# Performance work log

Hardware: AMD Instinct MI355X
Metric: run time of the kernel (lower is better)

The kernel has to match this reference:

```python
import jax, jax.numpy as jnp
import numpy as np
import math

N, T, NS, NO, HID = 256, 1000, 10, 10, 64


def gru_seq(x, Wi, Wh, bi, bh):
    # x: [N,T,D] -> hidden states [N,T,HID] (single-layer GRU, h0 = 0)
    xproj = x @ Wi + bi  # [N,T,3H], precompute input projections
    def step(h, xp):
        hp = h @ Wh + bh
        xr, xz, xn = jnp.split(xp, 3, axis=-1)
        hr, hz, hn = jnp.split(hp, 3, axis=-1)
        r = jax.nn.sigmoid(xr + hr)
        z = jax.nn.sigmoid(xz + hz)
        n = jnp.tanh(xn + r * hn)
        h_new = (1.0 - z) * n + z * h
        return h_new, h_new
    h0 = jnp.zeros((x.shape[0], Wh.shape[0]), x.dtype)
    _, hs = jax.lax.scan(step, h0, jnp.swapaxes(xproj, 0, 1))
    return jnp.swapaxes(hs, 0, 1)


def setup_inputs() -> dict:
    key = jax.random.key(0)
    ks = jax.random.split(key, 12)
    D = NO + NS  # GRU input = concat(y, x_hat)
    s = lambda fan: 1.0 / np.sqrt(fan)
    inp = {
        "Yi_batch": jax.random.normal(ks[0], (N, T, NO), jnp.float32),
        "X_hat_batch": jax.random.normal(ks[1], (N, T, NS), jnp.float32),
        # per-sample observation noise covariance: 0.5*I plus small random diagonal
        "Cw_batch": 0.5 * jnp.eye(NO, dtype=jnp.float32)[None] + jnp.eye(NO)[None] * 0.1 * jax.random.uniform(ks[2], (N, 1, 1), jnp.float32),
        "H": jax.random.normal(ks[3], (NO, NS), jnp.float32) * s(NS),
        "mu_w": jnp.zeros((NO, 1), jnp.float32),
        "Wi": jax.random.normal(ks[4], (D, 3 * HID), jnp.float32) * s(D),
        "Wh": jax.random.normal(ks[5], (HID, 3 * HID), jnp.float32) * s(HID),
        "bi": jnp.zeros((3 * HID,), jnp.float32),
        "bh": jnp.zeros((3 * HID,), jnp.float32),
        "W_mu": jax.random.normal(ks[6], (HID, NS), jnp.float32) * s(HID),
        "b_mu": jnp.zeros((NS,), jnp.float32),
        "W_var": jax.random.normal(ks[7], (HID, NS), jnp.float32) * s(HID),
        "b_var": jnp.zeros((NS,), jnp.float32),
    }
    return inp


def reference(Yi_batch, X_hat_batch, Cw_batch, H, mu_w, Wi, Wh, bi, bh, W_mu, b_mu, W_var, b_var):
    n_obs = Yi_batch.shape[-1]
    Tlen = Yi_batch.shape[1]
    # RNN: mu and (positive) vars per time step
    hs = gru_seq(jnp.concatenate([Yi_batch, X_hat_batch], axis=-1), Wi, Wh, bi, bh)
    mu_prev = hs @ W_mu + b_mu                       # [N,T,NS]
    var_prev = jax.nn.softplus(hs @ W_var + b_var)   # [N,T,NS] diag of L_xt_yt_prev
    # marginal over y: mu_y = H mu_prev + mu_w ; L_y = H diag(var) H^T + Cw
    mu_y = jnp.einsum('ij,ntj->nti', H, mu_prev) + mu_w[:, 0]
    HLH = jnp.einsum('ij,ntj,kj->ntik', H, var_prev, H)   # [N,T,NO,NO]
    L_y = HLH + Cw_batch[:, None]                          # broadcast Cw over time
    e = Yi_batch - mu_y
    # Gaussian log-likelihood via Cholesky (L_y is SPD)
    chol = jnp.linalg.cholesky(L_y)
    logdet = 2.0 * jnp.sum(jnp.log(jnp.diagonal(chol, axis1=-2, axis2=-1)), axis=-1)  # [N,T]
    sol = jnp.linalg.solve(L_y, e[..., None])[..., 0]
    quad = jnp.sum(e * sol, axis=-1)                       # [N,T]
    logprob = (-0.5 * n_obs * Tlen * math.log(2.0 * math.pi)
               - 0.5 * jnp.sum(logdet, axis=1)
               - 0.5 * jnp.sum(quad, axis=1))              # [N]
    return jnp.mean(logprob / (Tlen * n_obs))
```

## Files before the change

kernel.cpp:

```cpp
#include <hip/hip_runtime.h>
#include <math.h>

#define BN 256
#define TT 1000
#define NO 10
#define NS 10
#define HID 64
#define DIN 20
#define G3 192
#define WV 4
#define KW 16
#define GS 8
#define NG 125

__device__ __forceinline__ float bcast(float v, int l) {
    return __int_as_float(__builtin_amdgcn_readlane(__float_as_int(v), l));
}
__device__ __forceinline__ float rcpf(float x) { return __builtin_amdgcn_rcpf(x); }

__global__ __launch_bounds__(256, 1)
void gru_phase1(const float* __restrict__ Yi, const float* __restrict__ Xh,
                const float* __restrict__ Wi, const float* __restrict__ Wh,
                const float* __restrict__ bi, const float* __restrict__ bh,
                const float* __restrict__ Wmu, const float* __restrict__ Wvar,
                float* __restrict__ mv_out) {
    const int n = blockIdx.x;
    const int tid = threadIdx.x;
    const int lane = tid & 63;
    const int w = tid >> 6;
    const int kb = w * KW;

    __shared__ float part[2][5][WV][HID];
    __shared__ float inbuf[2][GS * DIN];
    __shared__ float obuf[2][GS * DIN];

    float whr[KW], whz[KW], whn[KW], wmv[KW];
    float wir[5], wiz[5], win[5];
#pragma unroll
    for (int k = 0; k < KW; ++k) {
        const int kk = kb + k;
        whr[k] = Wh[kk * G3 + lane];
        whz[k] = Wh[kk * G3 + 64 + lane];
        whn[k] = Wh[kk * G3 + 128 + lane];
        float wm = (lane < NS) ? Wmu[kk * NS + lane] : 0.0f;
        float wv = (lane >= NS && lane < 2 * NS) ? Wvar[kk * NS + (lane - NS)] : 0.0f;
        wmv[k] = wm + wv;
    }
#pragma unroll
    for (int k = 0; k < 5; ++k) {
        const int kk = 5 * w + k;
        wir[k] = Wi[kk * G3 + lane];
        wiz[k] = Wi[kk * G3 + 64 + lane];
        win[k] = Wi[kk * G3 + 128 + lane];
    }
    const float b_r  = bi[lane] + bh[lane];
    const float b_z  = bi[64 + lane] + bh[64 + lane];
    const float bx_n = bi[128 + lane];
    const float bh_n = bh[128 + lane];

    const float* ybase = Yi + (size_t)n * TT * NO;
    const float* xbase = Xh + (size_t)n * TT * NS;
    float* obase = mv_out + (size_t)n * TT * DIN;

    const int ibase = ((w >= 2) ? 80 : 0) + (w & 1) * 5;

    if (tid < 160)
        inbuf[0][tid] = (tid < 80) ? ybase[tid] : xbase[tid - 80];
    __syncthreads();

    float h = 0.0f;

#pragma unroll 1
    for (int g = 0; g < NG; ++g) {
        float ld = 0.0f;
        const bool do_ld = (tid < 160) && (g + 1 < NG);
        if (do_ld)
            ld = (tid < 80) ? ybase[(size_t)(g + 1) * 80 + tid]
                            : xbase[(size_t)(g + 1) * 80 + tid - 80];
        const float* ib = inbuf[g & 1];

#pragma unroll
        for (int s = 0; s < GS; ++s) {
            const float* ip = ib + ibase + s * 10;
            const float x0 = ip[0], x1 = ip[1], x2 = ip[2], x3 = ip[3], x4 = ip[4];
            float pr = x0 * wir[0], pz = x0 * wiz[0], px = x0 * win[0];
            pr += x1 * wir[1]; pz += x1 * wiz[1]; px += x1 * win[1];
            pr += x2 * wir[2]; pz += x2 * wiz[2]; px += x2 * win[2];
            pr += x3 * wir[3]; pz += x3 * wiz[3]; px += x3 * win[3];
            pr += x4 * wir[4]; pz += x4 * wiz[4]; px += x4 * win[4];
            float pra = 0, prb = 0, pza = 0, pzb = 0;
            float pna = 0, pnb = 0, pma = 0, pmb = 0;
#pragma unroll
            for (int k = 0; k < 8; ++k) {
                float sv = bcast(h, kb + k);
                pra += sv * whr[k]; pza += sv * whz[k];
                pna += sv * whn[k]; pma += sv * wmv[k];
            }
#pragma unroll
            for (int k = 8; k < KW; ++k) {
                float sv = bcast(h, kb + k);
                prb += sv * whr[k]; pzb += sv * whz[k];
                pnb += sv * whn[k]; pmb += sv * wmv[k];
            }
            const int bufp = s & 1;
            part[bufp][0][w][lane] = pr + pra + prb;
            part[bufp][1][w][lane] = pz + pza + pzb;
            part[bufp][2][w][lane] = px;
            part[bufp][3][w][lane] = pna + pnb;
            part[bufp][4][w][lane] = pma + pmb;
            if (s == GS - 1 && do_ld) inbuf[(g + 1) & 1][tid] = ld;
            __syncthreads();

            float ar = b_r, az = b_z, ax = bx_n, ah = bh_n;
#pragma unroll
            for (int ww = 0; ww < WV; ++ww) {
                ar += part[bufp][0][ww][lane];
                az += part[bufp][1][ww][lane];
                ax += part[bufp][2][ww][lane];
                ah += part[bufp][3][ww][lane];
            }
            if (w == 0) {
                float amv = part[bufp][4][0][lane] + part[bufp][4][1][lane]
                          + part[bufp][4][2][lane] + part[bufp][4][3][lane];
                if (lane < DIN && !(g == 0 && s == 0)) {
                    const int tm1 = 8 * g + s - 1;
                    obuf[(tm1 >> 3) & 1][(tm1 & 7) * DIN + lane] = amv;
                }
            }
            if (s == 1 && g >= 1 && tid < 160)
                obase[(size_t)(g - 1) * 160 + tid] = obuf[(g - 1) & 1][tid];

            float r = rcpf(1.0f + __expf(-ar));
            float z = rcpf(1.0f + __expf(-az));
            float pre = ax + r * ah;
            pre = fminf(fmaxf(pre, -15.0f), 15.0f);
            float e2 = __expf(2.0f * pre);
            float nn = 1.0f - 2.0f * rcpf(e2 + 1.0f);
            h = nn + z * (h - nn);
        }
    }

    {
        float pma = 0, pmb = 0;
#pragma unroll
        for (int k = 0; k < 8; ++k) pma += bcast(h, kb + k) * wmv[k];
#pragma unroll
        for (int k = 8; k < KW; ++k) pmb += bcast(h, kb + k) * wmv[k];
        part[0][4][w][lane] = pma + pmb;
        __syncthreads();
        if (w == 0 && lane < DIN) {
            float amv = part[0][4][0][lane] + part[0][4][1][lane]
                      + part[0][4][2][lane] + part[0][4][3][lane];
            obuf[0][7 * DIN + lane] = amv;
        }
        __syncthreads();
        if (tid < 160)
            obase[(size_t)(NG - 1) * 160 + tid] = obuf[0][tid];
    }
}

__global__ void init_out(float* out) {
    out[0] = -0.918938533204672742f;
}

__global__ __launch_bounds__(256)
void lik_phase2(const float* __restrict__ Yi, const float* __restrict__ Cw,
                const float* __restrict__ Hm, const float* __restrict__ mu_w,
                const float* __restrict__ b_mu, const float* __restrict__ b_var,
                const float* __restrict__ mv_in, float* __restrict__ out) {
    __shared__ float sH[NO * NS];
    __shared__ float smw[NO], sbm[NS], sbv[NS];
    __shared__ float ssum[4];
    const int tid = threadIdx.x;
    if (tid < NO * NS) sH[tid] = Hm[tid];
    if (tid < NO) smw[tid] = mu_w[tid];
    if (tid < NS) { sbm[tid] = b_mu[tid]; sbv[tid] = b_var[tid]; }
    __syncthreads();

    const int gid = blockIdx.x * 256 + tid;
    float contrib = 0.0f;
    if (gid < BN * TT) {
        const int n = gid / TT;
        const float* mv = mv_in + (size_t)gid * DIN;
        float mu[NS], va[NS];
#pragma unroll
        for (int i = 0; i < NS; ++i) {
            mu[i] = mv[i] + sbm[i];
            float x = mv[NS + i] + sbv[i];
            va[i] = (x > 0.0f) ? (x + log1pf(__expf(-x))) : log1pf(__expf(x));
        }
        const float* y = Yi + (size_t)gid * NO;
        float e[NO];
#pragma unroll
        for (int i = 0; i < NO; ++i) {
            float m = smw[i];
#pragma unroll
            for (int j = 0; j < NS; ++j) m += sH[i * NS + j] * mu[j];
            e[i] = y[i] - m;
        }
        float M[NO][NO];
        const float* cw = Cw + (size_t)n * NO * NO;
#pragma unroll
        for (int i = 0; i < NO; ++i)
#pragma unroll
            for (int j = 0; j <= i; ++j) M[i][j] = cw[i * NO + j];
#pragma unroll
        for (int l = 0; l < NS; ++l) {
            float vl = va[l];
            float hv[NO];
#pragma unroll
            for (int i = 0; i < NO; ++i) hv[i] = sH[i * NS + l];
#pragma unroll
            for (int i = 0; i < NO; ++i) {
                float hvi = hv[i] * vl;
#pragma unroll
                for (int j = 0; j <= i; ++j) M[i][j] += hvi * hv[j];
            }
        }
        float logdet = 0.0f;
#pragma unroll
        for (int j = 0; j < NO; ++j) {
            float d = M[j][j];
#pragma unroll
            for (int k = 0; k < j; ++k) d -= M[j][k] * M[j][k];
            logdet += __logf(d);
            float s = sqrtf(d);
            M[j][j] = s;
            float inv = 1.0f / s;
#pragma unroll
            for (int i = j + 1; i < NO; ++i) {
                float v = M[i][j];
#pragma unroll
                for (int k = 0; k < j; ++k) v -= M[i][k] * M[j][k];
                M[i][j] = v * inv;
            }
        }
        float wv[NO];
        float quad = 0.0f;
#pragma unroll
        for (int i = 0; i < NO; ++i) {
            float v = e[i];
#pragma unroll
            for (int k = 0; k < i; ++k) v -= M[i][k] * wv[k];
            wv[i] = v / M[i][i];
            quad += wv[i] * wv[i];
        }
        const float SCALE = 0.5f / ((float)BN * (float)TT * (float)NO);
        contrib = -(logdet + quad) * SCALE;
    }

#pragma unroll
    for (int off = 32; off > 0; off >>= 1) contrib += __shfl_down(contrib, off);
    if ((tid & 63) == 0) ssum[tid >> 6] = contrib;
    __syncthreads();
    if (tid == 0) {
        float s = ssum[0] + ssum[1] + ssum[2] + ssum[3];
        atomicAdd(out, s);
    }
}

extern "C" void kernel_launch(void* const* d_in, const int* in_sizes, int n_in,
                              void* d_out, int out_size, void* d_ws, size_t ws_size,
                              hipStream_t stream) {
    const float* Yi    = (const float*)d_in[0];
    const float* Xh    = (const float*)d_in[1];
    const float* Cw    = (const float*)d_in[2];
    const float* Hm    = (const float*)d_in[3];
    const float* mu_w  = (const float*)d_in[4];
    const float* Wi    = (const float*)d_in[5];
    const float* Wh    = (const float*)d_in[6];
    const float* bi    = (const float*)d_in[7];
    const float* bh    = (const float*)d_in[8];
    const float* W_mu  = (const float*)d_in[9];
    const float* b_mu  = (const float*)d_in[10];
    const float* W_var = (const float*)d_in[11];
    const float* b_var = (const float*)d_in[12];
    float* out = (float*)d_out;
    float* mv  = (float*)d_ws;

    init_out<<<1, 1, 0, stream>>>(out);
    gru_phase1<<<dim3(BN), dim3(256), 0, stream>>>(Yi, Xh, Wi, Wh, bi, bh,
                                                   W_mu, W_var, mv);
    lik_phase2<<<dim3((BN * TT + 255) / 256), dim3(256), 0, stream>>>(
        Yi, Cw, Hm, mu_w, b_mu, b_var, mv, out);
}
```

Before: 632.4 us.

## Pack two GRU samples per 512-thread block and drop tanh clamp

The GRU recurrence kernel now processes two batch samples per workgroup of 8 waves, giving 128 blocks instead of 256, with shared buffers indexed by sub-sample. The aim is to cut the block count so every block fits on the 256 CUs in a single wave, and to let two independent recurrences share each barrier and CU, hiding latency. The clamp on the tanh pre-activation is also removed. The risk is that each barrier now waits on 8 waves, which may lengthen the serial critical path per step. Without the clamp, a large pre-activation makes exp overflow to inf, which the rcp form still handles.

```diff
diff --git a/kernel.cpp b/kernel.cpp
--- a/kernel.cpp
+++ b/kernel.cpp
@@ -12,27 +12,38 @@
 #define KW 16
 #define GS 8
 #define NG 125
+#define SMP 2
 
 __device__ __forceinline__ float bcast(float v, int l) {
     return __int_as_float(__builtin_amdgcn_readlane(__float_as_int(v), l));
 }
 __device__ __forceinline__ float rcpf(float x) { return __builtin_amdgcn_rcpf(x); }
 
-__global__ __launch_bounds__(256, 1)
+__global__
+__attribute__((amdgpu_flat_work_group_size(512, 512), amdgpu_waves_per_eu(2, 2)))
 void gru_phase1(const float* __restrict__ Yi, const float* __restrict__ Xh,
                 const float* __restrict__ Wi, const float* __restrict__ Wh,
                 const float* __restrict__ bi, const float* __restrict__ bh,
                 const float* __restrict__ Wmu, const float* __restrict__ Wvar,
                 float* __restrict__ mv_out) {
-    const int n = blockIdx.x;
     const int tid = threadIdx.x;
     const int lane = tid & 63;
     const int w = tid >> 6;
-    const int kb = w * KW;
-
-    __shared__ float part[2][5][WV][HID];
-    __shared__ float inbuf[2][GS * DIN];
-    __shared__ float obuf[2][GS * DIN];
+    const int ws = w & 3;
+    const int sm = w >> 2;
+    const int kb = ws * KW;
+
+    __shared__ float part[2][5][SMP][WV][HID];
+    __shared__ float inbuf[2][SMP][GS * DIN];
+    __shared__ float obuf[2][SMP][GS * DIN];
+
+    const int sm2 = (tid >= 160) ? 1 : 0;
+    const int lt = tid - 160 * sm2;
+    const bool stg = (tid < 320);
+    const int ns = 2 * blockIdx.x + sm2;
+    const float* ybase = Yi + (size_t)ns * TT * NO;
+    const float* xbase = Xh + (size_t)ns * TT * NS;
+    float* obase = mv_out + (size_t)ns * TT * DIN;
 
     float whr[KW], whz[KW], whn[KW], wmv[KW];
     float wir[5], wiz[5], win[5];
@@ -48,7 +59,7 @@
     }
 #pragma unroll
     for (int k = 0; k < 5; ++k) {
-        const int kk = 5 * w + k;
+        const int kk = 5 * ws + k;
         wir[k] = Wi[kk * G3 + lane];
         wiz[k] = Wi[kk * G3 + 64 + lane];
         win[k] = Wi[kk * G3 + 128 + lane];
@@ -58,14 +69,10 @@
     const float bx_n = bi[128 + lane];
     const float bh_n = bh[128 + lane];
 
-    const float* ybase = Yi + (size_t)n * TT * NO;
-    const float* xbase = Xh + (size_t)n * TT * NS;
-    float* obase = mv_out + (size_t)n * TT * DIN;
-
-    const int ibase = ((w >= 2) ? 80 : 0) + (w & 1) * 5;
-
-    if (tid < 160)
-        inbuf[0][tid] = (tid < 80) ? ybase[tid] : xbase[tid - 80];
+    const int ibase = ((ws >= 2) ? 80 : 0) + (ws & 1) * 5;
+
+    if (stg)
+        inbuf[0][sm2][lt] = (lt < 80) ? ybase[lt] : xbase[lt - 80];
     __syncthreads();
 
     float h = 0.0f;
@@ -73,11 +80,11 @@
 #pragma unroll 1
     for (int g = 0; g < NG; ++g) {
         float ld = 0.0f;
-        const bool do_ld = (tid < 160) && (g + 1 < NG);
+        const bool do_ld = stg && (g + 1 < NG);
         if (do_ld)
-            ld = (tid < 80) ? ybase[(size_t)(g + 1) * 80 + tid]
-                            : xbase[(size_t)(g + 1) * 80 + tid - 80];
-        const float* ib = inbuf[g & 1];
+            ld = (lt < 80) ? ybase[(size_t)(g + 1) * 80 + lt]
+                           : xbase[(size_t)(g + 1) * 80 + (lt - 80)];
+        const float* ib = inbuf[g & 1][sm];
 
 #pragma unroll
         for (int s = 0; s < GS; ++s) {
@@ -103,37 +110,36 @@
                 pnb += sv * whn[k]; pmb += sv * wmv[k];
             }
             const int bufp = s & 1;
-            part[bufp][0][w][lane] = pr + pra + prb;
-            part[bufp][1][w][lane] = pz + pza + pzb;
-            part[bufp][2][w][lane] = px;
-            part[bufp][3][w][lane] = pna + pnb;
-            part[bufp][4][w][lane] = pma + pmb;
-            if (s == GS - 1 && do_ld) inbuf[(g + 1) & 1][tid] = ld;
+            part[bufp][0][sm][ws][lane] = pr + pra + prb;
+            part[bufp][1][sm][ws][lane] = pz + pza + pzb;
+            part[bufp][2][sm][ws][lane] = px;
+            part[bufp][3][sm][ws][lane] = pna + pnb;
+            part[bufp][4][sm][ws][lane] = pma + pmb;
+            if (s == GS - 1 && do_ld) inbuf[(g + 1) & 1][sm2][lt] = ld;
             __syncthreads();
 
             float ar = b_r, az = b_z, ax = bx_n, ah = bh_n;
 #pragma unroll
             for (int ww = 0; ww < WV; ++ww) {
-                ar += part[bufp][0][ww][lane];
-                az += part[bufp][1][ww][lane];
-                ax += part[bufp][2][ww][lane];
-                ah += part[bufp][3][ww][lane];
-            }
-            if (w == 0) {
-                float amv = part[bufp][4][0][lane] + part[bufp][4][1][lane]
-                          + part[bufp][4][2][lane] + part[bufp][4][3][lane];
+                ar += part[bufp][0][sm][ww][lane];
+                az += part[bufp][1][sm][ww][lane];
+                ax += part[bufp][2][sm][ww][lane];
+                ah += part[bufp][3][sm][ww][lane];
+            }
+            if (ws == 0) {
+                float amv = part[bufp][4][sm][0][lane] + part[bufp][4][sm][1][lane]
+                          + part[bufp][4][sm][2][lane] + part[bufp][4][sm][3][lane];
                 if (lane < DIN && !(g == 0 && s == 0)) {
                     const int tm1 = 8 * g + s - 1;
-                    obuf[(tm1 >> 3) & 1][(tm1 & 7) * DIN + lane] = amv;
+                    obuf[(tm1 >> 3) & 1][sm][(tm1 & 7) * DIN + lane] = amv;
                 }
             }
-            if (s == 1 && g >= 1 && tid < 160)
-                obase[(size_t)(g - 1) * 160 + tid] = obuf[(g - 1) & 1][tid];
+            if (s == 1 && g >= 1 && stg)
+                obase[(size_t)(g - 1) * 160 + lt] = obuf[(g - 1) & 1][sm2][lt];
 
             float r = rcpf(1.0f + __expf(-ar));
             float z = rcpf(1.0f + __expf(-az));
             float pre = ax + r * ah;
-            pre = fminf(fmaxf(pre, -15.0f), 15.0f);
             float e2 = __expf(2.0f * pre);
             float nn = 1.0f - 2.0f * rcpf(e2 + 1.0f);
             h = nn + z * (h - nn);
@@ -146,16 +152,16 @@
         for (int k = 0; k < 8; ++k) pma += bcast(h, kb + k) * wmv[k];
 #pragma unroll
         for (int k = 8; k < KW; ++k) pmb += bcast(h, kb + k) * wmv[k];
-        part[0][4][w][lane] = pma + pmb;
+        part[0][4][sm][ws][lane] = pma + pmb;
         __syncthreads();
-        if (w == 0 && lane < DIN) {
-            float amv = part[0][4][0][lane] + part[0][4][1][lane]
-                      + part[0][4][2][lane] + part[0][4][3][lane];
-            obuf[0][7 * DIN + lane] = amv;
+        if (ws == 0 && lane < DIN) {
+            float amv = part[0][4][sm][0][lane] + part[0][4][sm][1][lane]
+                      + part[0][4][sm][2][lane] + part[0][4][sm][3][lane];
+            obuf[0][sm][7 * DIN + lane] = amv;
         }
         __syncthreads();
-        if (tid < 160)
-            obase[(size_t)(NG - 1) * 160 + tid] = obuf[0][tid];
+        if (stg)
+            obase[(size_t)(NG - 1) * 160 + lt] = obuf[0][sm2][lt];
     }
 }
 
@@ -279,8 +285,8 @@
     float* mv  = (float*)d_ws;
 
     init_out<<<1, 1, 0, stream>>>(out);
-    gru_phase1<<<dim3(BN), dim3(256), 0, stream>>>(Yi, Xh, Wi, Wh, bi, bh,
-                                                   W_mu, W_var, mv);
+    gru_phase1<<<dim3(BN / SMP), dim3(512), 0, stream>>>(Yi, Xh, Wi, Wh, bi, bh,
+                                                         W_mu, W_var, mv);
     lik_phase2<<<dim3((BN * TT + 255) / 256), dim3(256), 0, stream>>>(
         Yi, Cw, Hm, mu_w, b_mu, b_var, mv, out);
 }
```

After: 886.3 us. 40.1% more time.

## Split GRU recurrence across eight waves and use lighter barrier and rsqrt

Applied to the files above, without the earlier changes.

The GRU kernel now runs 512 threads per block, so each of 8 waves handles 8 hidden units of the recurrent matmul and 2-3 input features instead of 16 and 5. This shortens the serial per-step FMA chain, at the cost of 8-way partial-sum reduction reads from LDS and a wider barrier. __syncthreads is replaced by a raw s_waitcnt plus s_barrier, and the tanh input clamp is dropped. The likelihood kernel switches to explicit fmaf and rsqrt-based Cholesky with reciprocal-based triangular solves.

```diff
diff --git a/kernel.cpp b/kernel.cpp
--- a/kernel.cpp
+++ b/kernel.cpp
@@ -8,8 +8,8 @@
 #define HID 64
 #define DIN 20
 #define G3 192
-#define WV 4
-#define KW 16
+#define WVS 8
+#define KW 8
 #define GS 8
 #define NG 125
 
@@ -18,24 +18,38 @@
 }
 __device__ __forceinline__ float rcpf(float x) { return __builtin_amdgcn_rcpf(x); }
 
-__global__ __launch_bounds__(256, 1)
+__device__ __forceinline__ void sync_lds() {
+    asm volatile("s_waitcnt lgkmcnt(0)\n\ts_barrier" ::: "memory");
+}
+
+__global__
+__attribute__((amdgpu_flat_work_group_size(512, 512), amdgpu_waves_per_eu(2, 2)))
 void gru_phase1(const float* __restrict__ Yi, const float* __restrict__ Xh,
                 const float* __restrict__ Wi, const float* __restrict__ Wh,
                 const float* __restrict__ bi, const float* __restrict__ bh,
                 const float* __restrict__ Wmu, const float* __restrict__ Wvar,
                 float* __restrict__ mv_out) {
-    const int n = blockIdx.x;
     const int tid = threadIdx.x;
     const int lane = tid & 63;
     const int w = tid >> 6;
     const int kb = w * KW;
 
-    __shared__ float part[2][5][WV][HID];
+    __shared__ float part[2][5][WVS][HID];
     __shared__ float inbuf[2][GS * DIN];
     __shared__ float obuf[2][GS * DIN];
 
+    const int n = blockIdx.x;
+    const float* ybase = Yi + (size_t)n * TT * NO;
+    const float* xbase = Xh + (size_t)n * TT * NS;
+    float* obase = mv_out + (size_t)n * TT * DIN;
+
+    const int dn = (w < 4) ? 3 : 2;
+    const int d0 = (w < 4) ? 3 * w : 12 + 2 * (w - 4);
+    const int ib0 = (d0 < 10) ? d0 : 70 + d0;
+    const int ib1 = (d0 + 1 < 10) ? d0 + 1 : 71 + d0;
+    const int ib2 = (dn == 3) ? ((d0 + 2 < 10) ? d0 + 2 : 72 + d0) : ib0;
+
     float whr[KW], whz[KW], whn[KW], wmv[KW];
-    float wir[5], wiz[5], win[5];
 #pragma unroll
     for (int k = 0; k < KW; ++k) {
         const int kk = kb + k;
@@ -46,27 +60,24 @@
         float wv = (lane >= NS && lane < 2 * NS) ? Wvar[kk * NS + (lane - NS)] : 0.0f;
         wmv[k] = wm + wv;
     }
-#pragma unroll
-    for (int k = 0; k < 5; ++k) {
-        const int kk = 5 * w + k;
-        wir[k] = Wi[kk * G3 + lane];
-        wiz[k] = Wi[kk * G3 + 64 + lane];
-        win[k] = Wi[kk * G3 + 128 + lane];
-    }
+    const float wir0 = Wi[d0 * G3 + lane];
+    const float wiz0 = Wi[d0 * G3 + 64 + lane];
+    const float win0 = Wi[d0 * G3 + 128 + lane];
+    const float wir1 = Wi[(d0 + 1) * G3 + lane];
+    const float wiz1 = Wi[(d0 + 1) * G3 + 64 + lane];
+    const float win1 = Wi[(d0 + 1) * G3 + 128 + lane];
+    const float wir2 = (dn == 3) ? Wi[(d0 + 2) * G3 + lane] : 0.0f;
+    const float wiz2 = (dn == 3) ? Wi[(d0 + 2) * G3 + 64 + lane] : 0.0f;
+    const float win2 = (dn == 3) ? Wi[(d0 + 2) * G3 + 128 + lane] : 0.0f;
+
     const float b_r  = bi[lane] + bh[lane];
     const float b_z  = bi[64 + lane] + bh[64 + lane];
     const float bx_n = bi[128 + lane];
     const float bh_n = bh[128 + lane];
 
-    const float* ybase = Yi + (size_t)n * TT * NO;
-    const float* xbase = Xh + (size_t)n * TT * NS;
-    float* obase = mv_out + (size_t)n * TT * DIN;
-
-    const int ibase = ((w >= 2) ? 80 : 0) + (w & 1) * 5;
-
     if (tid < 160)
         inbuf[0][tid] = (tid < 80) ? ybase[tid] : xbase[tid - 80];
-    __syncthreads();
+    sync_lds();
 
     float h = 0.0f;
 
@@ -76,52 +87,47 @@
         const bool do_ld = (tid < 160) && (g + 1 < NG);
         if (do_ld)
             ld = (tid < 80) ? ybase[(size_t)(g + 1) * 80 + tid]
-                            : xbase[(size_t)(g + 1) * 80 + tid - 80];
+                            : xbase[(size_t)(g + 1) * 80 + (tid - 80)];
         const float* ib = inbuf[g & 1];
 
 #pragma unroll
         for (int s = 0; s < GS; ++s) {
-            const float* ip = ib + ibase + s * 10;
-            const float x0 = ip[0], x1 = ip[1], x2 = ip[2], x3 = ip[3], x4 = ip[4];
-            float pr = x0 * wir[0], pz = x0 * wiz[0], px = x0 * win[0];
-            pr += x1 * wir[1]; pz += x1 * wiz[1]; px += x1 * win[1];
-            pr += x2 * wir[2]; pz += x2 * wiz[2]; px += x2 * win[2];
-            pr += x3 * wir[3]; pz += x3 * wiz[3]; px += x3 * win[3];
-            pr += x4 * wir[4]; pz += x4 * wiz[4]; px += x4 * win[4];
-            float pra = 0, prb = 0, pza = 0, pzb = 0;
-            float pna = 0, pnb = 0, pma = 0, pmb = 0;
-#pragma unroll
-            for (int k = 0; k < 8; ++k) {
+            const float x0 = ib[ib0 + 10 * s];
+            const float x1 = ib[ib1 + 10 * s];
+            const float x2 = ib[ib2 + 10 * s];
+            float pr = x0 * wir0, pz = x0 * wiz0, px = x0 * win0;
+            pr = fmaf(x1, wir1, pr); pz = fmaf(x1, wiz1, pz); px = fmaf(x1, win1, px);
+            pr = fmaf(x2, wir2, pr); pz = fmaf(x2, wiz2, pz); px = fmaf(x2, win2, px);
+            float pna = 0.0f, pma = 0.0f;
+#pragma unroll
+            for (int k = 0; k < KW; ++k) {
                 float sv = bcast(h, kb + k);
-                pra += sv * whr[k]; pza += sv * whz[k];
-                pna += sv * whn[k]; pma += sv * wmv[k];
-            }
-#pragma unroll
-            for (int k = 8; k < KW; ++k) {
-                float sv = bcast(h, kb + k);
-                prb += sv * whr[k]; pzb += sv * whz[k];
-                pnb += sv * whn[k]; pmb += sv * wmv[k];
+                pr  = fmaf(sv, whr[k], pr);
+                pz  = fmaf(sv, whz[k], pz);
+                pna = fmaf(sv, whn[k], pna);
+                pma = fmaf(sv, wmv[k], pma);
             }
             const int bufp = s & 1;
-            part[bufp][0][w][lane] = pr + pra + prb;
-            part[bufp][1][w][lane] = pz + pza + pzb;
+            part[bufp][0][w][lane] = pr;
+            part[bufp][1][w][lane] = pz;
             part[bufp][2][w][lane] = px;
-            part[bufp][3][w][lane] = pna + pnb;
-            part[bufp][4][w][lane] = pma + pmb;
+            part[bufp][3][w][lane] = pna;
+            part[bufp][4][w][lane] = pma;
             if (s == GS - 1 && do_ld) inbuf[(g + 1) & 1][tid] = ld;
-            __syncthreads();
+            sync_lds();
 
             float ar = b_r, az = b_z, ax = bx_n, ah = bh_n;
 #pragma unroll
-            for (int ww = 0; ww < WV; ++ww) {
+            for (int ww = 0; ww < WVS; ++ww) {
                 ar += part[bufp][0][ww][lane];
                 az += part[bufp][1][ww][lane];
                 ax += part[bufp][2][ww][lane];
                 ah += part[bufp][3][ww][lane];
             }
-            if (w == 0) {
-                float amv = part[bufp][4][0][lane] + part[bufp][4][1][lane]
-                          + part[bufp][4][2][lane] + part[bufp][4][3][lane];
+            if (w == 7) {
+                float amv = 0.0f;
+#pragma unroll
+                for (int ww = 0; ww < WVS; ++ww) amv += part[bufp][4][ww][lane];
                 if (lane < DIN && !(g == 0 && s == 0)) {
                     const int tm1 = 8 * g + s - 1;
                     obuf[(tm1 >> 3) & 1][(tm1 & 7) * DIN + lane] = amv;
@@ -133,7 +139,6 @@
             float r = rcpf(1.0f + __expf(-ar));
             float z = rcpf(1.0f + __expf(-az));
             float pre = ax + r * ah;
-            pre = fminf(fmaxf(pre, -15.0f), 15.0f);
             float e2 = __expf(2.0f * pre);
             float nn = 1.0f - 2.0f * rcpf(e2 + 1.0f);
             h = nn + z * (h - nn);
@@ -141,19 +146,18 @@
     }
 
     {
-        float pma = 0, pmb = 0;
-#pragma unroll
-        for (int k = 0; k < 8; ++k) pma += bcast(h, kb + k) * wmv[k];
-#pragma unroll
-        for (int k = 8; k < KW; ++k) pmb += bcast(h, kb + k) * wmv[k];
-        part[0][4][w][lane] = pma + pmb;
-        __syncthreads();
-        if (w == 0 && lane < DIN) {
-            float amv = part[0][4][0][lane] + part[0][4][1][lane]
-                      + part[0][4][2][lane] + part[0][4][3][lane];
+        float pma = 0.0f;
+#pragma unroll
+        for (int k = 0; k < KW; ++k) pma = fmaf(bcast(h, kb + k), wmv[k], pma);
+        part[0][4][w][lane] = pma;
+        sync_lds();
+        if (w == 7 && lane < DIN) {
+            float amv = 0.0f;
+#pragma unroll
+            for (int ww = 0; ww < WVS; ++ww) amv += part[0][4][ww][lane];
             obuf[0][7 * DIN + lane] = amv;
         }
-        __syncthreads();
+        sync_lds();
         if (tid < 160)
             obase[(size_t)(NG - 1) * 160 + tid] = obuf[0][tid];
     }
@@ -195,7 +199,7 @@
         for (int i = 0; i < NO; ++i) {
             float m = smw[i];
 #pragma unroll
-            for (int j = 0; j < NS; ++j) m += sH[i * NS + j] * mu[j];
+            for (int j = 0; j < NS; ++j) m = fmaf(sH[i * NS + j], mu[j], m);
             e[i] = y[i] - m;
         }
         float M[NO][NO];
@@ -214,25 +218,26 @@
             for (int i = 0; i < NO; ++i) {
                 float hvi = hv[i] * vl;
 #pragma unroll
-                for (int j = 0; j <= i; ++j) M[i][j] += hvi * hv[j];
+                for (int j = 0; j <= i; ++j) M[i][j] = fmaf(hvi, hv[j], M[i][j]);
             }
         }
         float logdet = 0.0f;
+        float drs[NO];
 #pragma unroll
         for (int j = 0; j < NO; ++j) {
             float d = M[j][j];
 #pragma unroll
-            for (int k = 0; k < j; ++k) d -= M[j][k] * M[j][k];
+            for (int k = 0; k < j; ++k) d = fmaf(-M[j][k], M[j][k], d);
             logdet += __logf(d);
-            float s = sqrtf(d);
-            M[j][j] = s;
-            float inv = 1.0f / s;
+            float rs = __frsqrt_rn(d);
+            drs[j] = rs;
+            M[j][j] = d * rs;
 #pragma unroll
             for (int i = j + 1; i < NO; ++i) {
                 float v = M[i][j];
 #pragma unroll
-                for (int k = 0; k < j; ++k) v -= M[i][k] * M[j][k];
-                M[i][j] = v * inv;
+                for (int k = 0; k < j; ++k) v = fmaf(-M[i][k], M[j][k], v);
+                M[i][j] = v * rs;
             }
         }
         float wv[NO];
@@ -241,9 +246,9 @@
         for (int i = 0; i < NO; ++i) {
             float v = e[i];
 #pragma unroll
-            for (int k = 0; k < i; ++k) v -= M[i][k] * wv[k];
-            wv[i] = v / M[i][i];
-            quad += wv[i] * wv[i];
+            for (int k = 0; k < i; ++k) v = fmaf(-M[i][k], wv[k], v);
+            wv[i] = v * drs[i] * rcpf(M[i][i] * drs[i]);
+            quad = fmaf(wv[i], wv[i], quad);
         }
         const float SCALE = 0.5f / ((float)BN * (float)TT * (float)NO);
         contrib = -(logdet + quad) * SCALE;
@@ -279,7 +284,7 @@
     float* mv  = (float*)d_ws;
 
     init_out<<<1, 1, 0, stream>>>(out);
-    gru_phase1<<<dim3(BN), dim3(256), 0, stream>>>(Yi, Xh, Wi, Wh, bi, bh,
+    gru_phase1<<<dim3(BN), dim3(512), 0, stream>>>(Yi, Xh, Wi, Wh, bi, bh,
                                                    W_mu, W_var, mv);
     lik_phase2<<<dim3((BN * TT + 255) / 256), dim3(256), 0, stream>>>(
         Yi, Cw, Hm, mu_w, b_mu, b_var, mv, out);
```

After: 809.2 us. 1.28x slower.
